# Kernel optimization log

Measured on AMD Instinct MI355X. Metric: run time of the kernel, lower is better.

## Reference

```python
import jax, jax.numpy as jnp
import numpy as np

N, D_IN, D_OUT = 10000, 256, 256


def setup_inputs() -> dict:
    key = jax.random.key(0)
    k1, k2, k3, k4 = jax.random.split(key, 4)
    # xavier_uniform with gain=1.414 (as in the torch module)
    def xavier(k, shape, gain=1.414):
        fan_in, fan_out = shape[0], shape[1]
        bound = gain * np.sqrt(6.0 / (fan_in + fan_out))
        return jax.random.uniform(k, shape, jnp.float32, -bound, bound)
    return {
        "input": jax.random.normal(k1, (N, D_IN), jnp.float32),
        "adj": jax.random.randint(k2, (N, N), 0, 2, jnp.int32),  # binary dense adjacency
        "M": N,
        "W": xavier(k3, (D_IN, D_OUT)),
        "b": jnp.zeros((D_OUT,), jnp.float32),
        "a": xavier(k4, (D_OUT, 1)),
    }


def reference(input, adj, M, W, b, a):
    # h = tanh(X W + b); values used for attention logits
    h = jnp.tanh(input @ W + b)          # [N, F]
    inp = input @ W                      # [N, F] (values to aggregate)
    e = (h @ a)[:, 0]                    # [N] per-node logit
    # original also drops neighbors whose h row sums to exactly 0
    valid = (jnp.sum(h, axis=1) != 0)    # [N]
    mask = (adj[:M] > 0) & valid[None, :]  # [M, N]
    neg = jnp.asarray(-1e30, h.dtype)
    scores = jnp.where(mask, e[None, :], neg)           # [M, N]
    m = jnp.max(scores, axis=1, keepdims=True)
    w = jnp.where(mask, jnp.exp(scores - m), 0.0)       # masked exp
    denom = jnp.sum(w, axis=1, keepdims=True)
    att = w / jnp.maximum(denom, 1e-30)  # rows with no neighbors -> all zeros (matches torch zeros init)
    # dropout is identity in eval mode (training=False)
    return att @ inp                     # [M, F]
```

## Files before the change

kernel.cpp:

```cpp
#include <hip/hip_runtime.h>
#include <hip/hip_bf16.h>
#include <cstdint>
#include <cstddef>

#define NN      10000
#define DD      256
#define KSTEP64 157
#define MB2     79
#define KSPLIT  6

typedef __bf16 bf16x8 __attribute__((ext_vector_type(8)));
typedef float  f32x4  __attribute__((ext_vector_type(4)));

#define XG_OFF   0ull
#define XG_SIZE  (32ull * 10000 * 16)
#define WG_OFF   (XG_OFF + XG_SIZE)
#define WG_SIZE  (32ull * 256 * 16)
#define INP_OFF  (WG_OFF + WG_SIZE)
#define INP_SIZE (10000ull * 256 * 4)
#define E_OFF    (INP_OFF + INP_SIZE)
#define E_SIZE   (10016ull * 4)
#define HS_OFF   (E_OFF + E_SIZE)
#define HS_SIZE  (10016ull * 4)
#define G_OFF    (HS_OFF + HS_SIZE)
#define G_SIZE   (10016ull * 4)
#define YG_OFF   (G_OFF + G_SIZE + 256ull)
#define YG_SIZE  (318ull * 1088 * 16)
#define PN_OFF   (YG_OFF + YG_SIZE)
#define PN_SIZE  ((size_t)KSPLIT * 10000 * 272 * 4)

__device__ __forceinline__ void gl_lds16(const void* g, void* lds) {
    __builtin_amdgcn_global_load_lds(
        (const __attribute__((address_space(1))) unsigned int*)g,
        (__attribute__((address_space(3))) unsigned int*)lds,
        16, 0, 0);
}

__global__ __launch_bounds__(256) void k_build_xg(const float* __restrict__ X,
                                                  bf16x8* __restrict__ XG) {
    int idx = blockIdx.x * 256 + threadIdx.x;
    int row = idx >> 5;
    int q   = idx & 31;
    const float* src = X + row * 256 + q * 8;
    bf16x8 v;
#pragma unroll
    for (int j = 0; j < 8; ++j) v[j] = (__bf16)src[j];
    XG[q * 10000 + row] = v;
}

__global__ __launch_bounds__(256) void k_build_wg(const float* __restrict__ W,
                                                  bf16x8* __restrict__ WG) {
    int e = blockIdx.x * 256 + threadIdx.x;
    int q = e >> 8;
    int n = e & 255;
    bf16x8 v;
#pragma unroll
    for (int j = 0; j < 8; ++j) v[j] = (__bf16)W[(q * 8 + j) * 256 + n];
    WG[e] = v;
}

__global__ __launch_bounds__(256) void k_gemm1(const bf16x8* __restrict__ XG,
                                               const bf16x8* __restrict__ WG,
                                               const float* __restrict__ bvec,
                                               const float* __restrict__ avec,
                                               float* __restrict__ inp,
                                               float* __restrict__ evec,
                                               float* __restrict__ hsumv) {
    __shared__ bf16x8 Ash[320];
    __shared__ bf16x8 Bsh[1024];
    __shared__ float ePart[4][80];
    __shared__ float hPart[4][80];
    int tid = threadIdx.x, wid = tid >> 6, lane = tid & 63;
    int l15 = lane & 15, l4 = lane >> 4;
    int mb = blockIdx.x;

    f32x4 acc[4][5];
#pragma unroll
    for (int c = 0; c < 4; ++c)
#pragma unroll
        for (int rt = 0; rt < 5; ++rt) acc[c][rt] = f32x4{0.f, 0.f, 0.f, 0.f};

    for (int kb = 0; kb < 8; ++kb) {
        for (int rr = wid; rr < 5; rr += 4) {
            int c = rr * 64 + lane;
            int g = c / 80, r = c - g * 80;
            gl_lds16(XG + ((kb * 4 + g) * 10000 + mb * 80 + r), (char*)Ash + rr * 1024);
        }
        for (int rr = wid; rr < 16; rr += 4)
            gl_lds16(WG + kb * 1024 + rr * 64 + lane, (char*)Bsh + rr * 1024);
        __syncthreads();

        bf16x8 af[5];
#pragma unroll
        for (int rt = 0; rt < 5; ++rt) af[rt] = Ash[l4 * 80 + rt * 16 + l15];
#pragma unroll
        for (int c = 0; c < 4; ++c) {
            bf16x8 bf = Bsh[l4 * 256 + (wid * 4 + c) * 16 + l15];
#pragma unroll
            for (int rt = 0; rt < 5; ++rt)
                acc[c][rt] = __builtin_amdgcn_mfma_f32_16x16x32_bf16(af[rt], bf, acc[c][rt], 0, 0, 0);
        }
        __syncthreads();
    }

    float pe[5][4], ph[5][4];
#pragma unroll
    for (int rt = 0; rt < 5; ++rt)
#pragma unroll
        for (int rg = 0; rg < 4; ++rg) { pe[rt][rg] = 0.f; ph[rt][rg] = 0.f; }

#pragma unroll
    for (int c = 0; c < 4; ++c) {
        int col = (wid * 4 + c) * 16 + l15;
        float av = avec[col];
        float bv = bvec[col];
#pragma unroll
        for (int rt = 0; rt < 5; ++rt) {
#pragma unroll
            for (int rg = 0; rg < 4; ++rg) {
                int row = mb * 80 + rt * 16 + l4 * 4 + rg;
                float v = acc[c][rt][rg];
                inp[row * 256 + col] = v;
                float h = tanhf(v + bv);
                pe[rt][rg] += h * av;
                ph[rt][rg] += h;
            }
        }
    }
#pragma unroll
    for (int rt = 0; rt < 5; ++rt) {
#pragma unroll
        for (int rg = 0; rg < 4; ++rg) {
            float se = pe[rt][rg], sh = ph[rt][rg];
#pragma unroll
            for (int m = 1; m < 16; m <<= 1) {
                se += __shfl_xor(se, m);
                sh += __shfl_xor(sh, m);
            }
            if (l15 == 0) {
                int lr = rt * 16 + l4 * 4 + rg;
                ePart[wid][lr] = se;
                hPart[wid][lr] = sh;
            }
        }
    }
    __syncthreads();
    if (tid < 80) {
        float e = ePart[0][tid] + ePart[1][tid] + ePart[2][tid] + ePart[3][tid];
        float h = hPart[0][tid] + hPart[1][tid] + hPart[2][tid] + hPart[3][tid];
        evec[mb * 80 + tid] = e;
        hsumv[mb * 80 + tid] = h;
    }
}

__global__ __launch_bounds__(1024) void k_softmax_g(const float* __restrict__ evec,
                                                    const float* __restrict__ hsumv,
                                                    float* __restrict__ gv) {
    __shared__ float red[1024];
    int tid = threadIdx.x;
    float m = -3.0e38f;
    for (int i = tid; i < NN; i += 1024)
        if (hsumv[i] != 0.0f) m = fmaxf(m, evec[i]);
    red[tid] = m;
    __syncthreads();
    for (int s = 512; s > 0; s >>= 1) {
        if (tid < s) red[tid] = fmaxf(red[tid], red[tid + s]);
        __syncthreads();
    }
    float gmax = red[0];
    if (gmax < -1.0e37f) gmax = 0.0f;
    for (int i = tid; i < 10016; i += 1024) {
        float g = 0.0f;
        if (i < NN && hsumv[i] != 0.0f) g = expf(evec[i] - gmax);
        gv[i] = g;
    }
}

__global__ __launch_bounds__(256) void k_build_yg(const float* __restrict__ inp,
                                                  const float* __restrict__ gv,
                                                  bf16x8* __restrict__ YG) {
    int kb = blockIdx.x;
    for (int c = threadIdx.x; c < 1088; c += 256) {
        int gq = c / 272, n = c - gq * 272;
        int k0 = kb * 32 + gq * 8;
        bf16x8 v;
#pragma unroll
        for (int j = 0; j < 8; ++j) {
            int k = k0 + j;
            float val = 0.0f;
            if (k < NN) {
                float gk = gv[k];
                if (n < 256) val = gk * inp[k * 256 + n];
                else if (n == 256) val = gk;
            }
            v[j] = (__bf16)val;
        }
        YG[kb * 1088 + c] = v;
    }
}

__device__ __forceinline__ bf16x8 cvt_adj(int4 a, int4 b) {
    union { bf16x8 v; unsigned int u[4]; } r;
    r.u[0] = (a.x > 0 ? 0x3F80u : 0u) | (a.y > 0 ? 0x3F800000u : 0u);
    r.u[1] = (a.z > 0 ? 0x3F80u : 0u) | (a.w > 0 ? 0x3F800000u : 0u);
    r.u[2] = (b.x > 0 ? 0x3F80u : 0u) | (b.y > 0 ? 0x3F800000u : 0u);
    r.u[3] = (b.z > 0 ? 0x3F80u : 0u) | (b.w > 0 ? 0x3F800000u : 0u);
    return r.v;
}

__global__ __launch_bounds__(256, 2) void k_attn_gemm(const int* __restrict__ adj,
                                                      const bf16x8* __restrict__ YG,
                                                      float* __restrict__ pnum) {
    __shared__ bf16x8 Bsh[2][2176];
    int tid = threadIdx.x, wid = tid >> 6, lane = tid & 63;
    int l15 = lane & 15, l4 = lane >> 4;
    int bid = blockIdx.x;
    int mb = bid / KSPLIT, kc = bid % KSPLIT;
    int s0 = (kc * KSTEP64) / KSPLIT, s1 = ((kc + 1) * KSTEP64) / KSPLIT;

    int mrow = mb * 128 + wid * 32 + l15;
    const int* pA = adj + (size_t)min(mrow, NN - 1) * 10000;
    const int* pB = adj + (size_t)min(mrow + 16, NN - 1) * 10000;
    int kgrp = l4 * 8;

    f32x4 acc[2][17];
#pragma unroll
    for (int t = 0; t < 2; ++t)
#pragma unroll
        for (int ct = 0; ct < 17; ++ct) acc[t][ct] = f32x4{0.f, 0.f, 0.f, 0.f};

    int4 aA[8], aB[8];

    auto stageB = [&](int sTile, int bufIdx) {
        const bf16x8* src = YG + (size_t)sTile * 2176;
        char* dst = (char*)&Bsh[bufIdx][0];
#pragma unroll
        for (int i = 0; i < 9; ++i) {
            int rr = wid + i * 4;
            if (rr < 34) gl_lds16(src + rr * 64 + lane, dst + rr * 1024);
        }
    };
    auto loadA = [&](int sTile, int4* dstA) {
        int kk0 = min(sTile * 64 + kgrp, 9992);
        int kk1 = min(sTile * 64 + 32 + kgrp, 9992);
        const int4* qa0 = (const int4*)(pA + kk0);
        const int4* qb0 = (const int4*)(pB + kk0);
        const int4* qa1 = (const int4*)(pA + kk1);
        const int4* qb1 = (const int4*)(pB + kk1);
        dstA[0] = qa0[0]; dstA[1] = qa0[1]; dstA[2] = qb0[0]; dstA[3] = qb0[1];
        dstA[4] = qa1[0]; dstA[5] = qa1[1]; dstA[6] = qb1[0]; dstA[7] = qb1[1];
    };
    auto compute = [&](bf16x8 f00, bf16x8 f01, bf16x8 f10, bf16x8 f11, int bufIdx) {
#pragma unroll
        for (int ct = 0; ct < 17; ++ct) {
            bf16x8 fb0 = Bsh[bufIdx][l4 * 272 + ct * 16 + l15];
            acc[0][ct] = __builtin_amdgcn_mfma_f32_16x16x32_bf16(f00, fb0, acc[0][ct], 0, 0, 0);
            acc[1][ct] = __builtin_amdgcn_mfma_f32_16x16x32_bf16(f01, fb0, acc[1][ct], 0, 0, 0);
            bf16x8 fb1 = Bsh[bufIdx][1088 + l4 * 272 + ct * 16 + l15];
            acc[0][ct] = __builtin_amdgcn_mfma_f32_16x16x32_bf16(f10, fb1, acc[0][ct], 0, 0, 0);
            acc[1][ct] = __builtin_amdgcn_mfma_f32_16x16x32_bf16(f11, fb1, acc[1][ct], 0, 0, 0);
        }
    };

    stageB(s0, 0);
    __builtin_amdgcn_sched_barrier(0);
    loadA(s0, aA);
    loadA(s0 + 1, aB);
    asm volatile("s_waitcnt vmcnt(16)" ::: "memory");
    __builtin_amdgcn_s_barrier();

    int s = s0, buf = 0;
#define K4_BODY(ASET)                                                          \
    {                                                                          \
        stageB(s + 1, buf ^ 1);                                                \
        __builtin_amdgcn_sched_barrier(0);                                     \
        bf16x8 f00 = cvt_adj(ASET[0], ASET[1]);                                \
        bf16x8 f01 = cvt_adj(ASET[2], ASET[3]);                                \
        bf16x8 f10 = cvt_adj(ASET[4], ASET[5]);                                \
        bf16x8 f11 = cvt_adj(ASET[6], ASET[7]);                                \
        loadA(s + 2, ASET);                                                    \
        __builtin_amdgcn_sched_barrier(0);                                     \
        compute(f00, f01, f10, f11, buf);                                      \
        asm volatile("s_waitcnt vmcnt(8)" ::: "memory");                       \
        __builtin_amdgcn_s_barrier();                                          \
        buf ^= 1; ++s;                                                         \
    }
    while (s + 2 <= s1) {
        K4_BODY(aA)
        K4_BODY(aB)
    }
#undef K4_BODY
    if (s < s1) {
        bf16x8 f00 = cvt_adj(aA[0], aA[1]);
        bf16x8 f01 = cvt_adj(aA[2], aA[3]);
        bf16x8 f10 = cvt_adj(aA[4], aA[5]);
        bf16x8 f11 = cvt_adj(aA[6], aA[7]);
        compute(f00, f01, f10, f11, buf);
    }

    float* base = pnum + (size_t)kc * 10000 * 272;
    int r0 = mb * 128 + wid * 32;
#pragma unroll
    for (int t = 0; t < 2; ++t) {
#pragma unroll
        for (int ct = 0; ct < 17; ++ct) {
            int col = ct * 16 + l15;
#pragma unroll
            for (int rg = 0; rg < 4; ++rg) {
                int row = r0 + t * 16 + l4 * 4 + rg;
                if (row < NN) base[(size_t)row * 272 + col] = acc[t][ct][rg];
            }
        }
    }
}

__global__ __launch_bounds__(256) void k_finalize(const float* __restrict__ pnum,
                                                  float* __restrict__ out) {
    int idx = blockIdx.x * 256 + threadIdx.x;
    int i = idx >> 6, q = idx & 63;
    float4 sv = {0.f, 0.f, 0.f, 0.f};
    float den = 0.f;
#pragma unroll
    for (int kc = 0; kc < KSPLIT; ++kc) {
        const float* row = pnum + ((size_t)kc * 10000 + i) * 272;
        float4 v = ((const float4*)row)[q];
        sv.x += v.x; sv.y += v.y; sv.z += v.z; sv.w += v.w;
        den += row[256];
    }
    float r = 1.0f / fmaxf(den, 1e-30f);
    float4 o;
    o.x = sv.x * r; o.y = sv.y * r; o.z = sv.z * r; o.w = sv.w * r;
    ((float4*)(out + (size_t)i * 256))[q] = o;
}

extern "C" void kernel_launch(void* const* d_in, const int* in_sizes, int n_in,
                              void* d_out, int out_size, void* d_ws, size_t ws_size,
                              hipStream_t stream) {
    const float* X    = (const float*)d_in[0];
    const int*   adj  = (const int*)d_in[1];
    const float* W    = (const float*)d_in[3];
    const float* bvec = (const float*)d_in[4];
    const float* avec = (const float*)d_in[5];
    float* out = (float*)d_out;

    char* ws = (char*)d_ws;
    bf16x8* XG   = (bf16x8*)(ws + XG_OFF);
    bf16x8* WG   = (bf16x8*)(ws + WG_OFF);
    float*  inp  = (float*)(ws + INP_OFF);
    float*  evec = (float*)(ws + E_OFF);
    float*  hsv  = (float*)(ws + HS_OFF);
    float*  gv   = (float*)(ws + G_OFF);
    bf16x8* YG   = (bf16x8*)(ws + YG_OFF);
    float*  pnum = (float*)(ws + PN_OFF);

    k_build_xg<<<1250, 256, 0, stream>>>(X, XG);
    k_build_wg<<<32, 256, 0, stream>>>(W, WG);
    k_gemm1<<<125, 256, 0, stream>>>(XG, WG, bvec, avec, inp, evec, hsv);
    k_softmax_g<<<1, 1024, 0, stream>>>(evec, hsv, gv);
    k_build_yg<<<318, 256, 0, stream>>>(inp, gv, YG);
    k_attn_gemm<<<MB2 * KSPLIT, 256, 0, stream>>>(adj, YG, pnum);
    k_finalize<<<2500, 256, 0, stream>>>(pnum, out);
}
```

Before: 195.3 us.

## Use 4-stage LDS ring with 32-wide K tiles and XCD-aware block remap

Halves the K tile of the adjacency-times-values GEMM to 32 and replaces the double buffer with a 4-slot LDS ring that prefetches three tiles ahead. The explicit vmcnt wait inside the loop is replaced by a plain compiler memory fence. Workgroup IDs are also remapped so that consecutive logical blocks, grouped by K-chunk, land on the same XCD, which should improve L2 reuse of the staged B tiles. The aim is to hide global-load latency behind the MFMA work. In exchange there are twice as many barriers per unit of work, and dropping the wait risks reading LDS slots before their asynchronous loads complete.

```diff
diff --git a/kernel.cpp b/kernel.cpp
--- a/kernel.cpp
+++ b/kernel.cpp
@@ -5,7 +5,7 @@
 
 #define NN      10000
 #define DD      256
-#define KSTEP64 157
+#define KSTEPS  313
 #define MB2     79
 #define KSPLIT  6
 
@@ -211,12 +211,16 @@
 __global__ __launch_bounds__(256, 2) void k_attn_gemm(const int* __restrict__ adj,
                                                       const bf16x8* __restrict__ YG,
                                                       float* __restrict__ pnum) {
-    __shared__ bf16x8 Bsh[2][2176];
+    __shared__ bf16x8 Bsh[4][1088];
     int tid = threadIdx.x, wid = tid >> 6, lane = tid & 63;
     int l15 = lane & 15, l4 = lane >> 4;
-    int bid = blockIdx.x;
-    int mb = bid / KSPLIT, kc = bid % KSPLIT;
-    int s0 = (kc * KSTEP64) / KSPLIT, s1 = ((kc + 1) * KSTEP64) / KSPLIT;
+
+    int orig = blockIdx.x;
+    const int nwg = MB2 * KSPLIT, q = nwg >> 3, r = nwg & 7;
+    int x = orig & 7, o = orig >> 3;
+    int logical = (x < r ? x * (q + 1) : r * (q + 1) + (x - r) * q) + o;
+    int kc = logical / MB2, mb = logical % MB2;
+    int s0 = (kc * KSTEPS) / KSPLIT, s1 = ((kc + 1) * KSTEPS) / KSPLIT;
 
     int mrow = mb * 128 + wid * 32 + l15;
     const int* pA = adj + (size_t)min(mrow, NN - 1) * 10000;
@@ -229,61 +233,54 @@
 #pragma unroll
         for (int ct = 0; ct < 17; ++ct) acc[t][ct] = f32x4{0.f, 0.f, 0.f, 0.f};
 
-    int4 aA[8], aB[8];
+    int4 aA[4], aB[4];
 
     auto stageB = [&](int sTile, int bufIdx) {
-        const bf16x8* src = YG + (size_t)sTile * 2176;
+        const bf16x8* src = YG + (size_t)sTile * 1088;
         char* dst = (char*)&Bsh[bufIdx][0];
 #pragma unroll
-        for (int i = 0; i < 9; ++i) {
+        for (int i = 0; i < 5; ++i) {
             int rr = wid + i * 4;
-            if (rr < 34) gl_lds16(src + rr * 64 + lane, dst + rr * 1024);
+            if (rr < 17) gl_lds16(src + rr * 64 + lane, dst + rr * 1024);
         }
     };
     auto loadA = [&](int sTile, int4* dstA) {
-        int kk0 = min(sTile * 64 + kgrp, 9992);
-        int kk1 = min(sTile * 64 + 32 + kgrp, 9992);
-        const int4* qa0 = (const int4*)(pA + kk0);
-        const int4* qb0 = (const int4*)(pB + kk0);
-        const int4* qa1 = (const int4*)(pA + kk1);
-        const int4* qb1 = (const int4*)(pB + kk1);
-        dstA[0] = qa0[0]; dstA[1] = qa0[1]; dstA[2] = qb0[0]; dstA[3] = qb0[1];
-        dstA[4] = qa1[0]; dstA[5] = qa1[1]; dstA[6] = qb1[0]; dstA[7] = qb1[1];
+        int kk = min(sTile * 32 + kgrp, 9992);
+        const int4* q0 = (const int4*)(pA + kk);
+        const int4* q1 = (const int4*)(pB + kk);
+        dstA[0] = q0[0]; dstA[1] = q0[1]; dstA[2] = q1[0]; dstA[3] = q1[1];
     };
-    auto compute = [&](bf16x8 f00, bf16x8 f01, bf16x8 f10, bf16x8 f11, int bufIdx) {
+    auto compute = [&](bf16x8 fa0, bf16x8 fa1, int bufIdx) {
 #pragma unroll
         for (int ct = 0; ct < 17; ++ct) {
-            bf16x8 fb0 = Bsh[bufIdx][l4 * 272 + ct * 16 + l15];
-            acc[0][ct] = __builtin_amdgcn_mfma_f32_16x16x32_bf16(f00, fb0, acc[0][ct], 0, 0, 0);
-            acc[1][ct] = __builtin_amdgcn_mfma_f32_16x16x32_bf16(f01, fb0, acc[1][ct], 0, 0, 0);
-            bf16x8 fb1 = Bsh[bufIdx][1088 + l4 * 272 + ct * 16 + l15];
-            acc[0][ct] = __builtin_amdgcn_mfma_f32_16x16x32_bf16(f10, fb1, acc[0][ct], 0, 0, 0);
-            acc[1][ct] = __builtin_amdgcn_mfma_f32_16x16x32_bf16(f11, fb1, acc[1][ct], 0, 0, 0);
+            bf16x8 fb = Bsh[bufIdx][l4 * 272 + ct * 16 + l15];
+            acc[0][ct] = __builtin_amdgcn_mfma_f32_16x16x32_bf16(fa0, fb, acc[0][ct], 0, 0, 0);
+            acc[1][ct] = __builtin_amdgcn_mfma_f32_16x16x32_bf16(fa1, fb, acc[1][ct], 0, 0, 0);
         }
     };
 
-    stageB(s0, 0);
+    stageB(s0,     (s0)     & 3);
+    stageB(s0 + 1, (s0 + 1) & 3);
+    stageB(s0 + 2, (s0 + 2) & 3);
     __builtin_amdgcn_sched_barrier(0);
     loadA(s0, aA);
     loadA(s0 + 1, aB);
-    asm volatile("s_waitcnt vmcnt(16)" ::: "memory");
+    asm volatile("s_waitcnt vmcnt(8)" ::: "memory");
     __builtin_amdgcn_s_barrier();
 
-    int s = s0, buf = 0;
+    int s = s0;
 #define K4_BODY(ASET)                                                          \
     {                                                                          \
-        stageB(s + 1, buf ^ 1);                                                \
+        stageB(s + 3, (s + 3) & 3);                                            \
         __builtin_amdgcn_sched_barrier(0);                                     \
-        bf16x8 f00 = cvt_adj(ASET[0], ASET[1]);                                \
-        bf16x8 f01 = cvt_adj(ASET[2], ASET[3]);                                \
-        bf16x8 f10 = cvt_adj(ASET[4], ASET[5]);                                \
-        bf16x8 f11 = cvt_adj(ASET[6], ASET[7]);                                \
+        bf16x8 fa0 = cvt_adj(ASET[0], ASET[1]);                                \
+        bf16x8 fa1 = cvt_adj(ASET[2], ASET[3]);                                \
         loadA(s + 2, ASET);                                                    \
         __builtin_amdgcn_sched_barrier(0);                                     \
-        compute(f00, f01, f10, f11, buf);                                      \
-        asm volatile("s_waitcnt vmcnt(8)" ::: "memory");                       \
+        compute(fa0, fa1, s & 3);                                              \
+        asm volatile("" ::: "memory");                                         \
         __builtin_amdgcn_s_barrier();                                          \
-        buf ^= 1; ++s;                                                         \
+        ++s;                                                                   \
     }
     while (s + 2 <= s1) {
         K4_BODY(aA)
@@ -291,11 +288,9 @@
     }
 #undef K4_BODY
     if (s < s1) {
-        bf16x8 f00 = cvt_adj(aA[0], aA[1]);
-        bf16x8 f01 = cvt_adj(aA[2], aA[3]);
-        bf16x8 f10 = cvt_adj(aA[4], aA[5]);
-        bf16x8 f11 = cvt_adj(aA[6], aA[7]);
-        compute(f00, f01, f10, f11, buf);
+        bf16x8 fa0 = cvt_adj(aA[0], aA[1]);
+        bf16x8 fa1 = cvt_adj(aA[2], aA[3]);
+        compute(fa0, fa1, s & 3);
     }
 
     float* base = pnum + (size_t)kc * 10000 * 272;
```

Result: slower. 203.6 us (+4.3%).
